# Performance work log

Measured on AMD Instinct MI355X. Metric: run time of the kernel, lower is better.

## Reference

```python
import jax, jax.numpy as jnp
import numpy as np

B, F, Q, DIM, H, DH, MULT = 16, 4096, 64, 512, 8, 64, 2
EPS = 1e-5


def _ln(x, g, b):
    m = jnp.mean(x, axis=-1, keepdims=True)
    v = jnp.mean(jnp.square(x - m), axis=-1, keepdims=True)
    return (x - m) * jax.lax.rsqrt(v + EPS) * g + b


def setup_inputs() -> dict:
    key = jax.random.key(0)
    ks = jax.random.split(key, 8)
    s = 0.02
    return {
        "features": jax.random.normal(ks[0], (B, F, DIM), jnp.float32),
        "latents": jax.random.normal(ks[1], (B, Q, DIM), jnp.float32),
        "mask": jax.random.randint(ks[2], (B, F), 0, 2, jnp.int32),
        "gf": jnp.ones((DIM,), jnp.float32),
        "bf": jnp.zeros((DIM,), jnp.float32),
        "gl": jnp.ones((DIM,), jnp.float32),
        "bl": jnp.zeros((DIM,), jnp.float32),
        "Wq": jax.random.normal(ks[3], (DIM, DIM), jnp.float32) * s,
        "Wk": jax.random.normal(ks[4], (DIM, DIM), jnp.float32) * s,
        "Wv": jax.random.normal(ks[5], (DIM, DIM), jnp.float32) * s,
        "gff": jnp.ones((DIM,), jnp.float32),
        "bff": jnp.zeros((DIM,), jnp.float32),
        "W1": jax.random.normal(ks[6], (DIM, MULT * DIM), jnp.float32) * s,
        "W2": jax.random.normal(ks[7], (MULT * DIM, DIM), jnp.float32) * s,
    }


def reference(features, latents, mask, gf, bf, gl, bl, Wq, Wk, Wv, gff, bff, W1, W2):
    scale = DH ** (-0.5)
    x = _ln(features, gf, bf)          # (B, F, DIM)
    lat = _ln(latents, gl, bl)         # (B, Q, DIM)
    q = (lat @ Wq).reshape(B, Q, H, DH).transpose(0, 2, 1, 3)  # b h q d
    k = (x @ Wk).reshape(B, F, H, DH).transpose(0, 2, 1, 3)    # b h f d
    v = (x @ Wv).reshape(B, F, H, DH).transpose(0, 2, 1, 3)    # b h f d
    sim = jnp.einsum('bhqd,bhfd->bhqf', q * scale, k)
    sim = sim - jax.lax.stop_gradient(jnp.max(sim, axis=-1, keepdims=True))
    sim = jnp.where(mask[:, None, None, :] == 0, -jnp.inf, sim)
    alphas = jnp.nan_to_num(jax.nn.softmax(sim, axis=-1), nan=0.0)
    out = jnp.einsum('bhqf,bhfd->bhqd', alphas, v)
    out = out.transpose(0, 2, 1, 3).reshape(B, Q, DIM)         # b q (h d)
    # feed-forward: LN -> Linear -> ReLU -> Linear (no bias)
    h = jax.nn.relu(_ln(out, gff, bff) @ W1)
    return h @ W2
```

## Files before the change

### kernel.cpp

```cpp
#include <hip/hip_runtime.h>
#include <hip/hip_bf16.h>
#include <math.h>

typedef short bf16x8 __attribute__((ext_vector_type(8)));
typedef float f32x4 __attribute__((ext_vector_type(4)));

__device__ __forceinline__ f32x4 mfma16(bf16x8 a, bf16x8 b, f32x4 c) {
    return __builtin_amdgcn_mfma_f32_16x16x32_bf16(a, b, c, 0, 0, 0);
}

__device__ __forceinline__ unsigned short f2b(float f) {
    unsigned int x = __float_as_uint(f);
    unsigned int r = (x + 0x7fffu + ((x >> 16) & 1u)) >> 16;
    return (unsigned short)r;
}

#define GLOBAL_AS(p) ((__attribute__((address_space(1))) void*)(p))
#define LDS_AS(p)    ((__attribute__((address_space(3))) void*)(p))

__global__ __launch_bounds__(64) void mask_compact(const int* __restrict__ mask,
                                                   int* __restrict__ cidx,
                                                   int* __restrict__ cntp) {
    int b = blockIdx.x;
    int lane = threadIdx.x;
    const int* mb = mask + b * 4096;
    int base = 0;
    for (int it = 0; it < 64; ++it) {
        int f = it * 64 + lane;
        int m = mb[f] != 0;
        unsigned long long bal = __ballot(m);
        int pre = __popcll(bal & ((1ull << lane) - 1ull));
        if (m) cidx[b * 4096 + base + pre] = f;
        base += __popcll(bal);
    }
    if (lane == 0) {
        cntp[b] = base;
        cntp[16 + b] = (base + 127) & ~127;
    }
}

__global__ __launch_bounds__(256) void ln_gather(const float* __restrict__ in,
                                                 const int* __restrict__ cidx,
                                                 const int* __restrict__ cntp,
                                                 const float* __restrict__ gw,
                                                 const float* __restrict__ bw,
                                                 unsigned short* __restrict__ out) {
    int row = blockIdx.x * 4 + (threadIdx.x >> 6);
    int lane = threadIdx.x & 63;
    int b = row >> 12, j = row & 4095;
    int cnt = cntp[b], padded = cntp[16 + b];
    if (j >= padded) return;
    unsigned short* orow = out + (size_t)row * 512;
    if (j >= cnt) {
        ushort4 z; z.x = z.y = z.z = z.w = 0;
        *(ushort4*)(orow + lane * 4) = z;
        *(ushort4*)(orow + 256 + lane * 4) = z;
        return;
    }
    int src = cidx[b * 4096 + j];
    const float* rp = in + ((size_t)b * 4096 + src) * 512;
    float4 x0 = *(const float4*)(rp + lane * 4);
    float4 x1 = *(const float4*)(rp + 256 + lane * 4);
    float s  = x0.x + x0.y + x0.z + x0.w + x1.x + x1.y + x1.z + x1.w;
    float sq = x0.x*x0.x + x0.y*x0.y + x0.z*x0.z + x0.w*x0.w
             + x1.x*x1.x + x1.y*x1.y + x1.z*x1.z + x1.w*x1.w;
#pragma unroll
    for (int m = 1; m < 64; m <<= 1) {
        s  += __shfl_xor(s, m);
        sq += __shfl_xor(sq, m);
    }
    float mean = s * (1.0f / 512.0f);
    float var  = sq * (1.0f / 512.0f) - mean * mean;
    float rs   = rsqrtf(var + 1e-5f);
    float4 g0 = *(const float4*)(gw + lane * 4);
    float4 g1 = *(const float4*)(gw + 256 + lane * 4);
    float4 b0 = *(const float4*)(bw + lane * 4);
    float4 b1 = *(const float4*)(bw + 256 + lane * 4);
    ushort4 o0, o1;
    o0.x = f2b((x0.x - mean) * rs * g0.x + b0.x);
    o0.y = f2b((x0.y - mean) * rs * g0.y + b0.y);
    o0.z = f2b((x0.z - mean) * rs * g0.z + b0.z);
    o0.w = f2b((x0.w - mean) * rs * g0.w + b0.w);
    o1.x = f2b((x1.x - mean) * rs * g1.x + b1.x);
    o1.y = f2b((x1.y - mean) * rs * g1.y + b1.y);
    o1.z = f2b((x1.z - mean) * rs * g1.z + b1.z);
    o1.w = f2b((x1.w - mean) * rs * g1.w + b1.w);
    *(ushort4*)(orow + lane * 4) = o0;
    *(ushort4*)(orow + 256 + lane * 4) = o1;
}

__global__ __launch_bounds__(256) void ln_rows(const float* __restrict__ in,
                                               const float* __restrict__ gw,
                                               const float* __restrict__ bw,
                                               unsigned short* __restrict__ out) {
    int row = blockIdx.x * 4 + (threadIdx.x >> 6);
    int lane = threadIdx.x & 63;
    const float* rp = in + (size_t)row * 512;
    float4 x0 = *(const float4*)(rp + lane * 4);
    float4 x1 = *(const float4*)(rp + 256 + lane * 4);
    float s  = x0.x + x0.y + x0.z + x0.w + x1.x + x1.y + x1.z + x1.w;
    float sq = x0.x*x0.x + x0.y*x0.y + x0.z*x0.z + x0.w*x0.w
             + x1.x*x1.x + x1.y*x1.y + x1.z*x1.z + x1.w*x1.w;
#pragma unroll
    for (int m = 1; m < 64; m <<= 1) {
        s  += __shfl_xor(s, m);
        sq += __shfl_xor(sq, m);
    }
    float mean = s * (1.0f / 512.0f);
    float var  = sq * (1.0f / 512.0f) - mean * mean;
    float rs   = rsqrtf(var + 1e-5f);
    float4 g0 = *(const float4*)(gw + lane * 4);
    float4 g1 = *(const float4*)(gw + 256 + lane * 4);
    float4 b0 = *(const float4*)(bw + lane * 4);
    float4 b1 = *(const float4*)(bw + 256 + lane * 4);
    ushort4 o0, o1;
    o0.x = f2b((x0.x - mean) * rs * g0.x + b0.x);
    o0.y = f2b((x0.y - mean) * rs * g0.y + b0.y);
    o0.z = f2b((x0.z - mean) * rs * g0.z + b0.z);
    o0.w = f2b((x0.w - mean) * rs * g0.w + b0.w);
    o1.x = f2b((x1.x - mean) * rs * g1.x + b1.x);
    o1.y = f2b((x1.y - mean) * rs * g1.y + b1.y);
    o1.z = f2b((x1.z - mean) * rs * g1.z + b1.z);
    o1.w = f2b((x1.w - mean) * rs * g1.w + b1.w);
    *(ushort4*)(out + (size_t)row * 512 + lane * 4) = o0;
    *(ushort4*)(out + (size_t)row * 512 + 256 + lane * 4) = o1;
}

__global__ __launch_bounds__(256) void transpose_all(const float* __restrict__ Wq,
                                                     const float* __restrict__ Wk,
                                                     const float* __restrict__ Wv,
                                                     const float* __restrict__ W1,
                                                     const float* __restrict__ W2,
                                                     unsigned short* __restrict__ WqT,
                                                     unsigned short* __restrict__ WkT,
                                                     unsigned short* __restrict__ WvT,
                                                     unsigned short* __restrict__ W1T,
                                                     unsigned short* __restrict__ W2T) {
    __shared__ float tile[32][33];
    int id = blockIdx.x;
    const float* in; unsigned short* out; int R, C;
    if (id < 256)       { in = Wq; out = WqT; R = 512;  C = 512;  }
    else if (id < 512)  { in = Wk; out = WkT; R = 512;  C = 512;  id -= 256;  }
    else if (id < 768)  { in = Wv; out = WvT; R = 512;  C = 512;  id -= 512;  }
    else if (id < 1280) { in = W1; out = W1T; R = 512;  C = 1024; id -= 768;  }
    else                { in = W2; out = W2T; R = 1024; C = 512;  id -= 1280; }
    int tilesX = C >> 5;
    int c0 = (id % tilesX) * 32, r0 = (id / tilesX) * 32;
    int tx = threadIdx.x & 31, ty = threadIdx.x >> 5;
#pragma unroll
    for (int i = 0; i < 32; i += 8)
        tile[ty + i][tx] = in[(size_t)(r0 + ty + i) * C + c0 + tx];
    __syncthreads();
#pragma unroll
    for (int i = 0; i < 32; i += 8)
        out[(size_t)(c0 + ty + i) * R + r0 + tx] = f2b(tile[tx][ty + i]);
}

template <int EPI>
__global__ __launch_bounds__(256) void gemm_bt(const unsigned short* __restrict__ A,
                                               const unsigned short* __restrict__ Bt,
                                               void* __restrict__ Cv,
                                               int M, int N, int K) {
    __shared__ unsigned short As[128 * 32];
    __shared__ unsigned short Bs[128 * 32];
    const int tid = threadIdx.x;
    const int wave = tid >> 6, lane = tid & 63;
    const int qd = lane >> 4, cc = lane & 15;
    const int m0 = blockIdx.y * 128, n0 = blockIdx.x * 128;
    const int wm = (wave >> 1) * 64, wn = (wave & 1) * 64;
    const int lrow = lane >> 2;
    const int lcol = (lane & 3) * 8;
    f32x4 acc[4][4] = {};

    for (int kt = 0; kt < K; kt += 32) {
#pragma unroll
        for (int r = 0; r < 2; ++r) {
            int slab = wave * 16 + r * 64;
            const unsigned short* ga = A + (size_t)(m0 + slab + lrow) * K + kt + lcol;
            __builtin_amdgcn_global_load_lds(GLOBAL_AS(ga), LDS_AS(&As[slab * 32]), 16, 0, 0);
            const unsigned short* gb = Bt + (size_t)(n0 + slab + lrow) * K + kt + lcol;
            __builtin_amdgcn_global_load_lds(GLOBAL_AS(gb), LDS_AS(&Bs[slab * 32]), 16, 0, 0);
        }
        __syncthreads();
        bf16x8 af[4], bfr[4];
#pragma unroll
        for (int i = 0; i < 4; ++i)
            af[i] = *(const bf16x8*)&As[(wm + i * 16 + cc) * 32 + qd * 8];
#pragma unroll
        for (int j = 0; j < 4; ++j)
            bfr[j] = *(const bf16x8*)&Bs[(wn + j * 16 + cc) * 32 + qd * 8];
#pragma unroll
        for (int i = 0; i < 4; ++i)
#pragma unroll
            for (int j = 0; j < 4; ++j)
                acc[i][j] = mfma16(af[i], bfr[j], acc[i][j]);
        __syncthreads();
    }
#pragma unroll
    for (int i = 0; i < 4; ++i) {
#pragma unroll
        for (int j = 0; j < 4; ++j) {
            int row = m0 + wm + i * 16 + qd * 4;
            int col = n0 + wn + j * 16 + cc;
#pragma unroll
            for (int r = 0; r < 4; ++r) {
                float v = acc[i][j][r];
                if (EPI == 1) v = fmaxf(v, 0.0f);
                if (EPI == 2)
                    ((float*)Cv)[(size_t)(row + r) * N + col] = v;
                else
                    ((unsigned short*)Cv)[(size_t)(row + r) * N + col] = f2b(v);
            }
        }
    }
}

__global__ __launch_bounds__(256, 2) void gemm_kv(const unsigned short* __restrict__ Xn,
                                                  const unsigned short* __restrict__ WkT,
                                                  const unsigned short* __restrict__ WvT,
                                                  const int* __restrict__ cntp,
                                                  unsigned short* __restrict__ Kout,
                                                  unsigned short* __restrict__ VTout) {
    const int L = blockIdx.x;
    const int t7 = L >> 3;
    const int c = t7 & 3;
    const int m = ((t7 >> 2) << 3) | (L & 7);
    const int m0 = m * 128;
    const int b = m0 >> 12;
    if ((m0 & 4095) >= cntp[16 + b]) return;
    __shared__ unsigned short Xs[128 * 32];
    __shared__ unsigned short Ks[128 * 32];
    __shared__ unsigned short Vs[128 * 32];
    const int tid = threadIdx.x;
    const int wave = tid >> 6, lane = tid & 63;
    const int qd = lane >> 4, cc = lane & 15;
    const int n0 = c * 128;
    const int wm = (wave >> 1) * 64, wn = (wave & 1) * 64;
    const int lrow = lane >> 2;
    const int lcol = (lane & 3) * 8;
    f32x4 accK[4][4] = {};
    f32x4 accV[4][4] = {};

    for (int kt = 0; kt < 512; kt += 32) {
#pragma unroll
        for (int r = 0; r < 2; ++r) {
            int slab = wave * 16 + r * 64;
            const unsigned short* gx = Xn + (size_t)(m0 + slab + lrow) * 512 + kt + lcol;
            __builtin_amdgcn_global_load_lds(GLOBAL_AS(gx), LDS_AS(&Xs[slab * 32]), 16, 0, 0);
            const unsigned short* gk = WkT + (size_t)(n0 + slab + lrow) * 512 + kt + lcol;
            __builtin_amdgcn_global_load_lds(GLOBAL_AS(gk), LDS_AS(&Ks[slab * 32]), 16, 0, 0);
            const unsigned short* gv = WvT + (size_t)(n0 + slab + lrow) * 512 + kt + lcol;
            __builtin_amdgcn_global_load_lds(GLOBAL_AS(gv), LDS_AS(&Vs[slab * 32]), 16, 0, 0);
        }
        __syncthreads();
        bf16x8 xf[4], kf[4], vf[4];
#pragma unroll
        for (int i = 0; i < 4; ++i)
            xf[i] = *(const bf16x8*)&Xs[(wm + i * 16 + cc) * 32 + qd * 8];
#pragma unroll
        for (int j = 0; j < 4; ++j) {
            kf[j] = *(const bf16x8*)&Ks[(wn + j * 16 + cc) * 32 + qd * 8];
            vf[j] = *(const bf16x8*)&Vs[(wn + j * 16 + cc) * 32 + qd * 8];
        }
#pragma unroll
        for (int i = 0; i < 4; ++i)
#pragma unroll
            for (int j = 0; j < 4; ++j) {
                accK[i][j] = mfma16(xf[i], kf[j], accK[i][j]);
                accV[j][i] = mfma16(vf[j], xf[i], accV[j][i]);
            }
        __syncthreads();
    }
#pragma unroll
    for (int i = 0; i < 4; ++i)
#pragma unroll
        for (int j = 0; j < 4; ++j) {
            int frow = (m0 & 4095) + wm + i * 16 + qd * 4;
            int dhg  = n0 + wn + j * 16 + cc;
            int hh = dhg >> 6, dhl = dhg & 63;
            unsigned short* kp = Kout + ((size_t)(b * 8 + hh) * 4096 + frow) * 64 + dhl;
#pragma unroll
            for (int r = 0; r < 4; ++r)
                kp[(size_t)r * 64] = f2b(accK[i][j][r]);
        }
#pragma unroll
    for (int j = 0; j < 4; ++j)
#pragma unroll
        for (int i = 0; i < 4; ++i) {
            int dhg = n0 + wn + j * 16 + qd * 4;
            int fg  = (m0 & 4095) + wm + i * 16 + cc;
            int hh = dhg >> 6, dhl = dhg & 63;
            unsigned short* vp = VTout + (size_t)(b * 8 + hh) * 262144
                               + (size_t)(fg >> 6) * 4096 + (size_t)dhl * 64 + (fg & 63);
#pragma unroll
            for (int r = 0; r < 4; ++r)
                vp[(size_t)r * 64] = f2b(accV[j][i][r]);
        }
}

__global__ __launch_bounds__(256, 3) void attn_kernel(const unsigned short* __restrict__ Qb,
                                                      const unsigned short* __restrict__ Khm,
                                                      const unsigned short* __restrict__ Vhm,
                                                      const int* __restrict__ cntp,
                                                      float* __restrict__ Opart,
                                                      float* __restrict__ lpart) {
    int blk = blockIdx.x;
    int b = blk >> 5;
    int h = (blk >> 2) & 7;
    int fs = blk & 3;
    int cnt = cntp[b];
    int pad = cntp[16 + b];
    int nchunks = pad >> 6;
    int wave = threadIdx.x >> 6, lane = threadIdx.x & 63;
    int qd = lane >> 4, cc = lane & 15;
    const int qt = wave;

    __shared__ unsigned short Ks[2][64 * 64];
    __shared__ unsigned short Vs[2][64 * 64];
    __shared__ unsigned short p_lds[4][16][72];

    const unsigned short* Kbase = Khm + (size_t)(b * 8 + h) * 262144;
    const unsigned short* Vbase = Vhm + (size_t)(b * 8 + h) * 262144;

    const unsigned short* qrow = Qb + (size_t)(b * 64 + qt * 16 + cc) * 512 + h * 64;
    bf16x8 qf0 = *(const bf16x8*)(qrow + qd * 8);
    bf16x8 qf1 = *(const bf16x8*)(qrow + 32 + qd * 8);
    bf16x8 ones;
#pragma unroll
    for (int j = 0; j < 8; ++j) ones[j] = (short)0x3F80;

    f32x4 O4[4] = {};
    f32x4 lac = {};
    const float cexp = 0.1803368801f;

#define STAGE(dst, cidx) do {                                                       \
        const char* kt_ = (const char*)(Kbase + (size_t)(cidx) * 4096);             \
        const char* vt_ = (const char*)(Vbase + (size_t)(cidx) * 4096);             \
        char* kd_ = (char*)&Ks[dst][0];                                             \
        char* vd_ = (char*)&Vs[dst][0];                                             \
        _Pragma("unroll")                                                           \
        for (int i_ = 0; i_ < 2; ++i_) {                                            \
            int o_ = i_ * 4096 + wave * 1024 + lane * 16;                           \
            int sb_ = o_ ^ (((o_ >> 7) & 7) << 4);                                  \
            __builtin_amdgcn_global_load_lds(GLOBAL_AS(kt_ + sb_),                  \
                LDS_AS(kd_ + i_ * 4096 + wave * 1024), 16, 0, 0);                   \
            __builtin_amdgcn_global_load_lds(GLOBAL_AS(vt_ + sb_),                  \
                LDS_AS(vd_ + i_ * 4096 + wave * 1024), 16, 0, 0);                   \
        }                                                                           \
    } while (0)

    int buf = 0;
    if (fs < nchunks) STAGE(0, fs);
    __syncthreads();

    const int swz = (cc & 7) << 4;
    for (int c = fs; c < nchunks; c += 4) {
        int cn = c + 4;
        if (cn < nchunks) STAGE(buf ^ 1, cn);

        const char* ksb = (const char*)&Ks[buf][0];
        const char* vsb = (const char*)&Vs[buf][0];
        int f0 = c * 64;
        bf16x8 kf[4][2], vf[4][2];
        int mv[4];
#pragma unroll
        for (int t = 0; t < 4; ++t) {
            int rb = (t * 16 + cc) * 128;
            kf[t][0] = *(const bf16x8*)(ksb + rb + ((qd << 4) ^ swz));
            kf[t][1] = *(const bf16x8*)(ksb + rb + ((64 + (qd << 4)) ^ swz));
            mv[t] = (f0 + t * 16 + cc) < cnt;
        }
#pragma unroll
        for (int g = 0; g < 4; ++g) {
            int rb = (g * 16 + cc) * 128;
            vf[g][0] = *(const bf16x8*)(vsb + rb + ((qd << 4) ^ swz));
            vf[g][1] = *(const bf16x8*)(vsb + rb + ((64 + (qd << 4)) ^ swz));
        }
        f32x4 s4[4] = {};
#pragma unroll
        for (int t = 0; t < 4; ++t) {
            s4[t] = mfma16(qf0, kf[t][0], s4[t]);
            s4[t] = mfma16(qf1, kf[t][1], s4[t]);
        }
#pragma unroll
        for (int t = 0; t < 4; ++t)
#pragma unroll
            for (int r = 0; r < 4; ++r) {
                float p = mv[t] ? exp2f(s4[t][r] * cexp) : 0.0f;
                p_lds[wave][qd * 4 + r][t * 16 + cc] = f2b(p);
            }
        bf16x8 pf0 = *(const bf16x8*)&p_lds[wave][cc][qd * 8];
        bf16x8 pf1 = *(const bf16x8*)&p_lds[wave][cc][32 + qd * 8];
        lac = mfma16(pf0, ones, lac);
        lac = mfma16(pf1, ones, lac);
#pragma unroll
        for (int g = 0; g < 4; ++g) {
            O4[g] = mfma16(pf0, vf[g][0], O4[g]);
            O4[g] = mfma16(pf1, vf[g][1], O4[g]);
        }
        __syncthreads();
        buf ^= 1;
    }
#undef STAGE

    float* op = Opart + (size_t)blk * 4096;
#pragma unroll
    for (int g = 0; g < 4; ++g)
#pragma unroll
        for (int r = 0; r < 4; ++r)
            op[(qt * 16 + qd * 4 + r) * 64 + g * 16 + cc] = O4[g][r];
    if (cc == 0) {
#pragma unroll
        for (int r = 0; r < 4; ++r)
            lpart[blk * 64 + qt * 16 + qd * 4 + r] = lac[r];
    }
}

__global__ __launch_bounds__(256) void ln_combine(const float* __restrict__ Opart,
                                                  const float* __restrict__ lpart,
                                                  const float* __restrict__ gw,
                                                  const float* __restrict__ bw,
                                                  unsigned short* __restrict__ out) {
    int row = blockIdx.x * 4 + (threadIdx.x >> 6);
    int lane = threadIdx.x & 63;
    int b = row >> 6, q = row & 63;
    int h = lane >> 3;
    int dh0 = (lane & 7) * 8;
    int blkbase = b * 32 + h * 4;
    float o[8] = {0,0,0,0,0,0,0,0};
    float l = 0.0f;
#pragma unroll
    for (int fsplit = 0; fsplit < 4; ++fsplit) {
        const float* op = Opart + (size_t)(blkbase + fsplit) * 4096 + q * 64 + dh0;
        float4 a0 = *(const float4*)op;
        float4 a1 = *(const float4*)(op + 4);
        o[0] += a0.x; o[1] += a0.y; o[2] += a0.z; o[3] += a0.w;
        o[4] += a1.x; o[5] += a1.y; o[6] += a1.z; o[7] += a1.w;
        l += lpart[(blkbase + fsplit) * 64 + q];
    }
    float inv = (l > 0.0f) ? 1.0f / l : 0.0f;
    float s = 0.0f, sq = 0.0f;
#pragma unroll
    for (int j = 0; j < 8; ++j) { o[j] *= inv; s += o[j]; sq += o[j] * o[j]; }
#pragma unroll
    for (int m = 1; m < 64; m <<= 1) {
        s  += __shfl_xor(s, m);
        sq += __shfl_xor(sq, m);
    }
    float mean = s * (1.0f / 512.0f);
    float var  = sq * (1.0f / 512.0f) - mean * mean;
    float rs   = rsqrtf(var + 1e-5f);
    int d0 = lane * 8;
    float4 g0 = *(const float4*)(gw + d0);
    float4 g1 = *(const float4*)(gw + d0 + 4);
    float4 b0 = *(const float4*)(bw + d0);
    float4 b1 = *(const float4*)(bw + d0 + 4);
    ushort4 w0, w1;
    w0.x = f2b((o[0] - mean) * rs * g0.x + b0.x);
    w0.y = f2b((o[1] - mean) * rs * g0.y + b0.y);
    w0.z = f2b((o[2] - mean) * rs * g0.z + b0.z);
    w0.w = f2b((o[3] - mean) * rs * g0.w + b0.w);
    w1.x = f2b((o[4] - mean) * rs * g1.x + b1.x);
    w1.y = f2b((o[5] - mean) * rs * g1.y + b1.y);
    w1.z = f2b((o[6] - mean) * rs * g1.z + b1.z);
    w1.w = f2b((o[7] - mean) * rs * g1.w + b1.w);
    *(ushort4*)(out + (size_t)row * 512 + d0) = w0;
    *(ushort4*)(out + (size_t)row * 512 + d0 + 4) = w1;
}

extern "C" void kernel_launch(void* const* d_in, const int* in_sizes, int n_in,
                              void* d_out, int out_size, void* d_ws, size_t ws_size,
                              hipStream_t stream) {
    const float* features = (const float*)d_in[0];
    const float* latents  = (const float*)d_in[1];
    const int*   mask     = (const int*)d_in[2];
    const float* gf  = (const float*)d_in[3];
    const float* bf_ = (const float*)d_in[4];
    const float* gl  = (const float*)d_in[5];
    const float* bl  = (const float*)d_in[6];
    const float* Wq  = (const float*)d_in[7];
    const float* Wk  = (const float*)d_in[8];
    const float* Wv  = (const float*)d_in[9];
    const float* gff = (const float*)d_in[10];
    const float* bff = (const float*)d_in[11];
    const float* W1  = (const float*)d_in[12];
    const float* W2  = (const float*)d_in[13];

    char* ws = (char*)d_ws;
    unsigned short* xn   = (unsigned short*)(ws);
    unsigned short* Kbuf = (unsigned short*)(ws + 67108864ull);
    unsigned short* VTb  = (unsigned short*)(ws + 134217728ull);
    unsigned short* latn = (unsigned short*)(ws + 201326592ull);
    unsigned short* Qbuf = (unsigned short*)(ws + 202375168ull);
    unsigned short* ffin = (unsigned short*)(ws + 205520896ull);
    unsigned short* hbuf = (unsigned short*)(ws + 206569472ull);
    unsigned short* WqT  = (unsigned short*)(ws + 208666624ull);
    unsigned short* WkT  = (unsigned short*)(ws + 209190912ull);
    unsigned short* WvT  = (unsigned short*)(ws + 209715200ull);
    unsigned short* W1T  = (unsigned short*)(ws + 210239488ull);
    unsigned short* W2T  = (unsigned short*)(ws + 211288064ull);
    int* cidx = (int*)(ws + 212336640ull);
    int* cntp = (int*)(ws + 212598784ull);
    float* Opart = (float*)(ws);
    float* lpart = (float*)(ws + 8388608ull);

    mask_compact<<<16, 64, 0, stream>>>(mask, cidx, cntp);

    transpose_all<<<1792, 256, 0, stream>>>(Wq, Wk, Wv, W1, W2, WqT, WkT, WvT, W1T, W2T);

    ln_gather<<<16384, 256, 0, stream>>>(features, cidx, cntp, gf, bf_, xn);
    ln_rows<<<256, 256, 0, stream>>>(latents, gl, bl, latn);

    gemm_kv<<<2048, 256, 0, stream>>>(xn, WkT, WvT, cntp, Kbuf, VTb);
    gemm_bt<0><<<dim3(4, 8), 256, 0, stream>>>(latn, WqT, Qbuf, 1024, 512, 512);

    attn_kernel<<<512, 256, 0, stream>>>(Qbuf, Kbuf, VTb, cntp, Opart, lpart);
    ln_combine<<<256, 256, 0, stream>>>(Opart, lpart, gff, bff, ffin);

    gemm_bt<1><<<dim3(8, 8), 256, 0, stream>>>(ffin, W1T, hbuf, 1024, 1024, 512);
    gemm_bt<2><<<dim3(4, 8), 256, 0, stream>>>(hbuf, W2T, (float*)d_out, 1024, 512, 1024);
}
```

Before: 366.3 us.

## Parallelize mask compaction, merge LayerNorm kernels, shrink small GEMM tiles

```diff
diff --git a/kernel.cpp b/kernel.cpp
--- a/kernel.cpp
+++ b/kernel.cpp
@@ -18,47 +18,82 @@
 #define GLOBAL_AS(p) ((__attribute__((address_space(1))) void*)(p))
 #define LDS_AS(p)    ((__attribute__((address_space(3))) void*)(p))
 
-__global__ __launch_bounds__(64) void mask_compact(const int* __restrict__ mask,
-                                                   int* __restrict__ cidx,
-                                                   int* __restrict__ cntp) {
+__global__ __launch_bounds__(1024) void mask_compact(const int* __restrict__ mask,
+                                                     int* __restrict__ cidx,
+                                                     int* __restrict__ cntp) {
+    __shared__ unsigned long long bals[64];
+    __shared__ int base[64];
     int b = blockIdx.x;
-    int lane = threadIdx.x;
+    int tid = threadIdx.x;
+    int wave = tid >> 6, lane = tid & 63;
     const int* mb = mask + b * 4096;
-    int base = 0;
-    for (int it = 0; it < 64; ++it) {
-        int f = it * 64 + lane;
-        int m = mb[f] != 0;
+#pragma unroll
+    for (int k = 0; k < 4; ++k) {
+        int g = wave * 4 + k;
+        int m = mb[g * 64 + lane] != 0;
         unsigned long long bal = __ballot(m);
+        if (lane == 0) bals[g] = bal;
+    }
+    __syncthreads();
+    if (wave == 0) {
+        int v = __popcll(bals[lane]);
+        int own = v;
+#pragma unroll
+        for (int off = 1; off < 64; off <<= 1) {
+            int n = __shfl_up(v, off);
+            if (lane >= off) v += n;
+        }
+        base[lane] = v - own;
+        if (lane == 63) {
+            cntp[b] = v;
+            cntp[16 + b] = (v + 127) & ~127;
+        }
+    }
+    __syncthreads();
+#pragma unroll
+    for (int k = 0; k < 4; ++k) {
+        int g = wave * 4 + k;
+        unsigned long long bal = bals[g];
+        int m = (int)((bal >> lane) & 1ull);
         int pre = __popcll(bal & ((1ull << lane) - 1ull));
-        if (m) cidx[b * 4096 + base + pre] = f;
-        base += __popcll(bal);
-    }
-    if (lane == 0) {
-        cntp[b] = base;
-        cntp[16 + b] = (base + 127) & ~127;
-    }
-}
-
-__global__ __launch_bounds__(256) void ln_gather(const float* __restrict__ in,
-                                                 const int* __restrict__ cidx,
-                                                 const int* __restrict__ cntp,
-                                                 const float* __restrict__ gw,
-                                                 const float* __restrict__ bw,
-                                                 unsigned short* __restrict__ out) {
-    int row = blockIdx.x * 4 + (threadIdx.x >> 6);
+        if (m) cidx[b * 4096 + base[g] + pre] = g * 64 + lane;
+    }
+}
+
+__global__ __launch_bounds__(256) void ln_all(const float* __restrict__ feat,
+                                              const float* __restrict__ lat,
+                                              const int* __restrict__ cidx,
+                                              const int* __restrict__ cntp,
+                                              const float* __restrict__ gf,
+                                              const float* __restrict__ bf_,
+                                              const float* __restrict__ gl,
+                                              const float* __restrict__ bl,
+                                              unsigned short* __restrict__ xn,
+                                              unsigned short* __restrict__ latn) {
+    int bid = blockIdx.x;
     int lane = threadIdx.x & 63;
-    int b = row >> 12, j = row & 4095;
-    int cnt = cntp[b], padded = cntp[16 + b];
-    if (j >= padded) return;
-    unsigned short* orow = out + (size_t)row * 512;
-    if (j >= cnt) {
-        ushort4 z; z.x = z.y = z.z = z.w = 0;
-        *(ushort4*)(orow + lane * 4) = z;
-        *(ushort4*)(orow + 256 + lane * 4) = z;
-        return;
-    }
-    int src = cidx[b * 4096 + j];
-    const float* rp = in + ((size_t)b * 4096 + src) * 512;
+    const float* rp; unsigned short* orow; const float *gw, *bw;
+    if (bid < 16384) {
+        int row = bid * 4 + (threadIdx.x >> 6);
+        int b = row >> 12, j = row & 4095;
+        int cnt = cntp[b], padded = cntp[16 + b];
+        if (j >= padded) return;
+        orow = xn + (size_t)row * 512;
+        if (j >= cnt) {
+            ushort4 z; z.x = z.y = z.z = z.w = 0;
+            *(ushort4*)(orow + lane * 4) = z;
+            *(ushort4*)(orow + 256 + lane * 4) = z;
+            return;
+        }
+        int src = cidx[b * 4096 + j];
+        rp = feat + ((size_t)b * 4096 + src) * 512;
+        gw = gf; bw = bf_;
+    } else {
+        int row = (bid - 16384) * 4 + (threadIdx.x >> 6);
+        rp = lat + (size_t)row * 512;
+        orow = latn + (size_t)row * 512;
+        gw = gl; bw = bl;
+    }
     float4 x0 = *(const float4*)(rp + lane * 4);
     float4 x1 = *(const float4*)(rp + 256 + lane * 4);
     float s  = x0.x + x0.y + x0.z + x0.w + x1.x + x1.y + x1.z + x1.w;
@@ -87,43 +122,6 @@
     o1.w = f2b((x1.w - mean) * rs * g1.w + b1.w);
     *(ushort4*)(orow + lane * 4) = o0;
     *(ushort4*)(orow + 256 + lane * 4) = o1;
-}
-
-__global__ __launch_bounds__(256) void ln_rows(const float* __restrict__ in,
-                                               const float* __restrict__ gw,
-                                               const float* __restrict__ bw,
-                                               unsigned short* __restrict__ out) {
-    int row = blockIdx.x * 4 + (threadIdx.x >> 6);
-    int lane = threadIdx.x & 63;
-    const float* rp = in + (size_t)row * 512;
-    float4 x0 = *(const float4*)(rp + lane * 4);
-    float4 x1 = *(const float4*)(rp + 256 + lane * 4);
-    float s  = x0.x + x0.y + x0.z + x0.w + x1.x + x1.y + x1.z + x1.w;
-    float sq = x0.x*x0.x + x0.y*x0.y + x0.z*x0.z + x0.w*x0.w
-             + x1.x*x1.x + x1.y*x1.y + x1.z*x1.z + x1.w*x1.w;
-#pragma unroll
-    for (int m = 1; m < 64; m <<= 1) {
-        s  += __shfl_xor(s, m);
-        sq += __shfl_xor(sq, m);
-    }
-    float mean = s * (1.0f / 512.0f);
-    float var  = sq * (1.0f / 512.0f) - mean * mean;
-    float rs   = rsqrtf(var + 1e-5f);
-    float4 g0 = *(const float4*)(gw + lane * 4);
-    float4 g1 = *(const float4*)(gw + 256 + lane * 4);
-    float4 b0 = *(const float4*)(bw + lane * 4);
-    float4 b1 = *(const float4*)(bw + 256 + lane * 4);
-    ushort4 o0, o1;
-    o0.x = f2b((x0.x - mean) * rs * g0.x + b0.x);
-    o0.y = f2b((x0.y - mean) * rs * g0.y + b0.y);
-    o0.z = f2b((x0.z - mean) * rs * g0.z + b0.z);
-    o0.w = f2b((x0.w - mean) * rs * g0.w + b0.w);
-    o1.x = f2b((x1.x - mean) * rs * g1.x + b1.x);
-    o1.y = f2b((x1.y - mean) * rs * g1.y + b1.y);
-    o1.z = f2b((x1.z - mean) * rs * g1.z + b1.z);
-    o1.w = f2b((x1.w - mean) * rs * g1.w + b1.w);
-    *(ushort4*)(out + (size_t)row * 512 + lane * 4) = o0;
-    *(ushort4*)(out + (size_t)row * 512 + 256 + lane * 4) = o1;
 }
 
 __global__ __launch_bounds__(256) void transpose_all(const float* __restrict__ Wq,
@@ -157,49 +155,45 @@
 }
 
 template <int EPI>
-__global__ __launch_bounds__(256) void gemm_bt(const unsigned short* __restrict__ A,
-                                               const unsigned short* __restrict__ Bt,
-                                               void* __restrict__ Cv,
-                                               int M, int N, int K) {
-    __shared__ unsigned short As[128 * 32];
-    __shared__ unsigned short Bs[128 * 32];
+__global__ __launch_bounds__(256) void gemm_bt64(const unsigned short* __restrict__ A,
+                                                 const unsigned short* __restrict__ Bt,
+                                                 void* __restrict__ Cv,
+                                                 int M, int N, int K) {
+    __shared__ unsigned short As[64 * 32];
+    __shared__ unsigned short Bs[64 * 32];
     const int tid = threadIdx.x;
     const int wave = tid >> 6, lane = tid & 63;
     const int qd = lane >> 4, cc = lane & 15;
-    const int m0 = blockIdx.y * 128, n0 = blockIdx.x * 128;
-    const int wm = (wave >> 1) * 64, wn = (wave & 1) * 64;
-    const int lrow = lane >> 2;
+    const int m0 = blockIdx.y * 64, n0 = blockIdx.x * 64;
+    const int wm = (wave >> 1) * 32, wn = (wave & 1) * 32;
+    const int lrow = wave * 16 + (lane >> 2);
     const int lcol = (lane & 3) * 8;
-    f32x4 acc[4][4] = {};
+    f32x4 acc[2][2] = {};
 
     for (int kt = 0; kt < K; kt += 32) {
-#pragma unroll
-        for (int r = 0; r < 2; ++r) {
-            int slab = wave * 16 + r * 64;
-            const unsigned short* ga = A + (size_t)(m0 + slab + lrow) * K + kt + lcol;
-            __builtin_amdgcn_global_load_lds(GLOBAL_AS(ga), LDS_AS(&As[slab * 32]), 16, 0, 0);
-            const unsigned short* gb = Bt + (size_t)(n0 + slab + lrow) * K + kt + lcol;
-            __builtin_amdgcn_global_load_lds(GLOBAL_AS(gb), LDS_AS(&Bs[slab * 32]), 16, 0, 0);
-        }
+        const unsigned short* ga = A + (size_t)(m0 + lrow) * K + kt + lcol;
+        __builtin_amdgcn_global_load_lds(GLOBAL_AS(ga), LDS_AS(&As[wave * 512]), 16, 0, 0);
+        const unsigned short* gb = Bt + (size_t)(n0 + lrow) * K + kt + lcol;
+        __builtin_amdgcn_global_load_lds(GLOBAL_AS(gb), LDS_AS(&Bs[wave * 512]), 16, 0, 0);
         __syncthreads();
-        bf16x8 af[4], bfr[4];
-#pragma unroll
-        for (int i = 0; i < 4; ++i)
+        bf16x8 af[2], bfr[2];
+#pragma unroll
+        for (int i = 0; i < 2; ++i)
             af[i] = *(const bf16x8*)&As[(wm + i * 16 + cc) * 32 + qd * 8];
 #pragma unroll
-        for (int j = 0; j < 4; ++j)
+        for (int j = 0; j < 2; ++j)
             bfr[j] = *(const bf16x8*)&Bs[(wn + j * 16 + cc) * 32 + qd * 8];
 #pragma unroll
-        for (int i = 0; i < 4; ++i)
-#pragma unroll
-            for (int j = 0; j < 4; ++j)
+        for (int i = 0; i < 2; ++i)
+#pragma unroll
+            for (int j = 0; j < 2; ++j)
                 acc[i][j] = mfma16(af[i], bfr[j], acc[i][j]);
         __syncthreads();
     }
 #pragma unroll
-    for (int i = 0; i < 4; ++i) {
-#pragma unroll
-        for (int j = 0; j < 4; ++j) {
+    for (int i = 0; i < 2; ++i) {
+#pragma unroll
+        for (int j = 0; j < 2; ++j) {
             int row = m0 + wm + i * 16 + qd * 4;
             int col = n0 + wn + j * 16 + cc;
 #pragma unroll
@@ -504,19 +498,19 @@
     float* Opart = (float*)(ws);
     float* lpart = (float*)(ws + 8388608ull);
 
-    mask_compact<<<16, 64, 0, stream>>>(mask, cidx, cntp);
+    mask_compact<<<16, 1024, 0, stream>>>(mask, cidx, cntp);
 
     transpose_all<<<1792, 256, 0, stream>>>(Wq, Wk, Wv, W1, W2, WqT, WkT, WvT, W1T, W2T);
 
-    ln_gather<<<16384, 256, 0, stream>>>(features, cidx, cntp, gf, bf_, xn);
-    ln_rows<<<256, 256, 0, stream>>>(latents, gl, bl, latn);
+    ln_all<<<16640, 256, 0, stream>>>(features, latents, cidx, cntp,
+                                      gf, bf_, gl, bl, xn, latn);
 
     gemm_kv<<<2048, 256, 0, stream>>>(xn, WkT, WvT, cntp, Kbuf, VTb);
-    gemm_bt<0><<<dim3(4, 8), 256, 0, stream>>>(latn, WqT, Qbuf, 1024, 512, 512);
+    gemm_bt64<0><<<dim3(8, 16), 256, 0, stream>>>(latn, WqT, Qbuf, 1024, 512, 512);
 
     attn_kernel<<<512, 256, 0, stream>>>(Qbuf, Kbuf, VTb, cntp, Opart, lpart);
     ln_combine<<<256, 256, 0, stream>>>(Opart, lpart, gff, bff, ffin);
 
-    gemm_bt<1><<<dim3(8, 8), 256, 0, stream>>>(ffin, W1T, hbuf, 1024, 1024, 512);
-    gemm_bt<2><<<dim3(4, 8), 256, 0, stream>>>(hbuf, W2T, (float*)d_out, 1024, 512, 1024);
-}
+    gemm_bt64<1><<<dim3(16, 16), 256, 0, stream>>>(ffin, W1T, hbuf, 1024, 1024, 512);
+    gemm_bt64<2><<<dim3(8, 16), 256, 0, stream>>>(hbuf, W2T, (float*)d_out, 1024, 512, 1024);
+}
```

After: 325.0 us. -11.3%, faster.
